# Optimization experiments

Measured on AMD Instinct MI355X. Metric: run time of the kernel, lower is better.

## Reference

```python
import jax, jax.numpy as jnp
import numpy as np

NUM_BINS = 16
BOUND = 3.0
MIN_BIN_WIDTH = 0.001
MIN_BIN_HEIGHT = 0.001
MIN_DERIVATIVE = 0.001
MIN_LAMBDA = 0.025
EPS = 1e-06


def setup_inputs() -> dict:
    key = jax.random.key(0)
    k1, k2 = jax.random.split(key)
    inputs = jax.random.normal(k1, (16384, 64), dtype=jnp.float32)
    params_unnorm = jax.random.normal(k2, (16384, 64, 4 * NUM_BINS - 1), dtype=jnp.float32)
    return {"inputs": inputs, "params_unnorm": params_unnorm}


def _calculate_knots(lengths, lower, upper):
    knots = jnp.cumsum(lengths, axis=-1) * (upper - lower) + lower
    pad = jnp.full(knots.shape[:-1] + (1,), lower, dtype=knots.dtype)
    knots = jnp.concatenate([pad, knots], axis=-1)
    knots = knots.at[..., -1].set(upper)
    lengths = jnp.diff(knots, axis=-1)
    return lengths, knots


def _spline_forward(inputs, params_unnorm):
    K = NUM_BINS
    w, h, d, lam = jnp.split(params_unnorm, [K, 2 * K, 3 * K - 1], axis=-1)
    w = jax.nn.softmax(w, axis=-1)
    h = jax.nn.softmax(h, axis=-1)
    d = jax.nn.softplus(d)
    lam = jax.nn.sigmoid(lam)

    widths = MIN_BIN_WIDTH + (1.0 - MIN_BIN_WIDTH * K) * w
    heights = MIN_BIN_HEIGHT + (1.0 - MIN_BIN_HEIGHT * K) * h
    derivatives = MIN_DERIVATIVE + d
    lambdas = (1.0 - 2.0 * MIN_LAMBDA) * lam + MIN_LAMBDA

    widths, cumwidths = _calculate_knots(widths, -BOUND, BOUND)
    heights, cumheights = _calculate_knots(heights, -BOUND, BOUND)
    # pad derivatives on both sides with 1 - min_derivative (boundary slopes == 1 after +min_derivative math in torch code semantics)
    edge = jnp.full(derivatives.shape[:-1] + (1,), 1.0 - MIN_DERIVATIVE, dtype=derivatives.dtype)
    derivatives = jnp.concatenate([edge, derivatives, edge], axis=-1)  # [..., K+1]

    # bin search: searchsorted(cumwidths + eps, x, right=True) - 1
    bin_idx = jnp.sum((cumwidths + EPS) <= inputs[..., None], axis=-1) - 1
    idx = jnp.clip(bin_idx, 0, K - 1)[..., None]

    def sel(x):
        return jnp.take_along_axis(x, idx, axis=-1)[..., 0]

    input_widths = sel(widths)
    input_heights = sel(heights)
    input_delta = input_heights / input_widths
    input_cumwidths = sel(cumwidths)
    input_cumheights = sel(cumheights)
    input_derivatives = sel(derivatives)
    input_derivatives_plus_one = sel(derivatives[..., 1:])
    input_lambdas = sel(lambdas)

    wb = jnp.sqrt(input_derivatives / input_derivatives_plus_one)
    lwa = input_lambdas
    lwb = input_lambdas * wb
    wc = (lwa * input_derivatives + (wb - lwb) * input_derivatives_plus_one) / input_delta
    ya = input_cumheights
    yb = input_heights + input_cumheights
    l1 = 1.0 - input_lambdas
    yc = (lwb * yb + l1 * ya) / (l1 + lwb)

    waya = ya
    wbyb = wb * yb
    wcyc = wc * yc
    theta = (inputs - input_cumwidths) / input_widths
    indicator = theta <= input_lambdas
    ltheta = input_lambdas - theta
    wcyctheta = wcyc * theta
    numerator = jnp.where(indicator, wcyctheta + waya * ltheta, (wcyc - wcyctheta) - wbyb * ltheta)
    wctheta = wc * theta
    denominator = jnp.where(indicator, wctheta + ltheta, (wc - wctheta) - wb * ltheta)
    outputs = numerator / denominator
    derivative_numerator = wc * jnp.where(
        indicator, input_lambdas * (yc - ya), (wb - lwb) * (yb - yc)
    ) / input_widths
    logabsdet = jnp.log(derivative_numerator) - 2.0 * jnp.log(jnp.abs(denominator))

    outside = (inputs < -BOUND) | (inputs > BOUND)
    outputs = jnp.where(outside, inputs, outputs)
    logabsdet = jnp.where(outside, 0.0, logabsdet)
    return outputs, logabsdet


def reference(inputs, params_unnorm):
    return _spline_forward(inputs, params_unnorm)
```

## Files before the change

### kernel.cpp

```cpp
#include <hip/hip_runtime.h>
#include <math.h>

#define NBINS 16
#define BOUNDV 3.0f
#define MIN_W 0.001f
#define MIN_H 0.001f
#define MIN_D 0.001f
#define MIN_L 0.025f
#define EPSV 1e-6f

#define TPB 128
#define PPE 63
#define SLABDW (TPB * PPE)
#define NVEC (SLABDW / 4)
#define TAILV (NVEC - 15 * TPB)

__device__ __forceinline__ float frcp(float v) { return __builtin_amdgcn_rcpf(v); }

__device__ __forceinline__ void load_slab(float4* v, const float* __restrict__ params,
                                          int s, int tid) {
    const float4* __restrict__ src = (const float4*)(params + (size_t)s * SLABDW);
    #pragma unroll
    for (int k = 0; k < 15; ++k) v[k] = src[tid + k * TPB];
    if (tid < TAILV) v[15] = src[tid + 15 * TPB];
}

__device__ __forceinline__ void store_slab(float* b, int tid, const float4* v) {
    float4* dst = (float4*)b;
    #pragma unroll
    for (int k = 0; k < 15; ++k) dst[tid + k * TPB] = v[k];
    if (tid < TAILV) dst[tid + 15 * TPB] = v[15];
}

__global__ __launch_bounds__(TPB) void lrs_kernel(
    const float* __restrict__ x_in,
    const float* __restrict__ params,
    float* __restrict__ out,
    int n)
{
    __shared__ __align__(16) float buf0[SLABDW];
    __shared__ __align__(16) float buf1[SLABDW];
    const int tid = threadIdx.x;
    const int nslab = n / TPB;
    const int g = gridDim.x;

    int s = blockIdx.x;
    if (s >= nslab) return;

    float4 v[16];
    load_slab(v, params, s, tid);
    float xc = x_in[(size_t)s * TPB + tid];
    store_slab(buf0, tid, v);
    __syncthreads();

    float* cur = buf0;
    float* nxt = buf1;

    for (; s < nslab; s += g) {
        const int sn = s + g;
        const bool hn = (sn < nslab);
        float xn = 0.f;
        if (hn) {
            load_slab(v, params, sn, tid);
            xn = x_in[(size_t)sn * TPB + tid];
        }

        const float* p = cur + tid * PPE;
        const float x = xc;

        float wv[NBINS];
        float mw = -1e30f;
        #pragma unroll
        for (int i = 0; i < NBINS; ++i) { wv[i] = p[i]; mw = fmaxf(mw, wv[i]); }
        float sw = 0.f;
        #pragma unroll
        for (int i = 0; i < NBINS; ++i) { wv[i] = __expf(wv[i] - mw); sw += wv[i]; }
        const float invw = frcp(sw);

        float cum = 0.f, knp = -BOUNDV, cw = -BOUNDV, cwn = 0.f;
        int bin = 0;
        #pragma unroll
        for (int i = 0; i < NBINS; ++i) {
            cum += fmaf(0.984f, wv[i] * invw, MIN_W);
            float kn = (i == NBINS - 1) ? BOUNDV : fmaf(6.f, cum, -BOUNDV);
            bool hit = (knp + EPSV <= x);
            if (i == 0) { cwn = kn; }
            else if (hit) { bin = i; cw = knp; cwn = kn; }
            knp = kn;
        }

        const float draw_lo = p[31 + bin];
        const float draw_hi = p[32 + bin];
        const float lraw    = p[47 + bin];

        float hv[NBINS];
        float mh = -1e30f;
        #pragma unroll
        for (int i = 0; i < NBINS; ++i) { hv[i] = p[16 + i]; mh = fmaxf(mh, hv[i]); }
        float sh = 0.f;
        #pragma unroll
        for (int i = 0; i < NBINS; ++i) { hv[i] = __expf(hv[i] - mh); sh += hv[i]; }
        const float invh = frcp(sh);

        float cumh = 0.f, khp = -BOUNDV, ya = -BOUNDV, yb = 0.f;
        #pragma unroll
        for (int i = 0; i < NBINS; ++i) {
            cumh += fmaf(0.984f, hv[i] * invh, MIN_H);
            float kh = (i == NBINS - 1) ? BOUNDV : fmaf(6.f, cumh, -BOUNDV);
            if (i == bin) { ya = khp; yb = kh; }
            khp = kh;
        }

        const float sp_lo = fmaxf(draw_lo, 0.f) + __logf(1.f + __expf(-fabsf(draw_lo)));
        const float sp_hi = fmaxf(draw_hi, 0.f) + __logf(1.f + __expf(-fabsf(draw_hi)));
        const float d_k  = (bin == 0)         ? (1.f - MIN_D) : (MIN_D + sp_lo);
        const float d_k1 = (bin == NBINS - 1) ? (1.f - MIN_D) : (MIN_D + sp_hi);

        const float sig = frcp(1.f + __expf(-lraw));
        const float lam = fmaf(1.f - 2.f * MIN_L, sig, MIN_L);

        const float width  = cwn - cw;
        const float height = yb - ya;
        const float inv_w  = frcp(width);
        const float inv_dl = width * frcp(height);

        const float wb  = __builtin_amdgcn_sqrtf(d_k * frcp(d_k1));
        const float lwb = lam * wb;
        const float wc  = (lam * d_k + (wb - lwb) * d_k1) * inv_dl;
        const float l1  = 1.f - lam;
        const float yc  = (lwb * yb + l1 * ya) * frcp(l1 + lwb);

        const float theta = (x - cw) * inv_w;
        const bool  ind   = (theta <= lam);
        const float lt    = lam - theta;

        const float wcyc  = wc * yc;
        const float wcyct = wcyc * theta;
        const float num   = ind ? fmaf(ya, lt, wcyct)
                                : (wcyc - wcyct) - (wb * yb) * lt;
        const float wct   = wc * theta;
        const float den   = ind ? (wct + lt)
                                : (wc - wct) - wb * lt;
        float outv = num * frcp(den);

        const float dnum = wc * (ind ? lam * (yc - ya) : (wb - lwb) * (yb - yc)) * inv_w;
        float lad = __logf(dnum) - 2.f * __logf(fabsf(den));

        const bool outside = (x < -BOUNDV) | (x > BOUNDV);
        outv = outside ? x   : outv;
        lad  = outside ? 0.f : lad;

        const size_t gid = (size_t)s * TPB + tid;
        out[gid]     = outv;
        out[n + gid] = lad;

        if (hn) store_slab(nxt, tid, v);
        __syncthreads();
        float* t = cur; cur = nxt; nxt = t;
        xc = xn;
    }
}

extern "C" void kernel_launch(void* const* d_in, const int* in_sizes, int n_in,
                              void* d_out, int out_size, void* d_ws, size_t ws_size,
                              hipStream_t stream) {
    const float* x      = (const float*)d_in[0];
    const float* params = (const float*)d_in[1];
    float* out          = (float*)d_out;
    const int n = in_sizes[0];
    const int blocks = 512;
    lrs_kernel<<<blocks, TPB, 0, stream>>>(x, params, out, n);
}
```

Baseline: 400.5 us.

## Use direct global-to-LDS loads and one-slab-per-block grid instead of persistent double buffering

The persistent double-buffered loop is replaced by a kernel that launches one block per 128-element slab. Each block copies its parameters straight from global memory into LDS with global_load_lds, skipping the register staging pass. The goal is more memory-level parallelism from many resident blocks and no register pressure from the float4 staging array. In exchange there is no explicit overlap inside a block, which relies on occupancy across blocks, and the LDS destination addressing of the wave-wide load intrinsic must be exactly right.

```diff
diff --git a/kernel.cpp b/kernel.cpp
--- a/kernel.cpp
+++ b/kernel.cpp
@@ -11,26 +11,14 @@
 
 #define TPB 128
 #define PPE 63
-#define SLABDW (TPB * PPE)
-#define NVEC (SLABDW / 4)
-#define TAILV (NVEC - 15 * TPB)
+#define NVEC (TPB * PPE / 4)
 
 __device__ __forceinline__ float frcp(float v) { return __builtin_amdgcn_rcpf(v); }
 
-__device__ __forceinline__ void load_slab(float4* v, const float* __restrict__ params,
-                                          int s, int tid) {
-    const float4* __restrict__ src = (const float4*)(params + (size_t)s * SLABDW);
-    #pragma unroll
-    for (int k = 0; k < 15; ++k) v[k] = src[tid + k * TPB];
-    if (tid < TAILV) v[15] = src[tid + 15 * TPB];
-}
-
-__device__ __forceinline__ void store_slab(float* b, int tid, const float4* v) {
-    float4* dst = (float4*)b;
-    #pragma unroll
-    for (int k = 0; k < 15; ++k) dst[tid + k * TPB] = v[k];
-    if (tid < TAILV) dst[tid + 15 * TPB] = v[15];
-}
+#define GLOAD_LDS16(gp, lp)                                             \
+    __builtin_amdgcn_global_load_lds(                                   \
+        (const __attribute__((address_space(1))) void*)(gp),            \
+        (__attribute__((address_space(3))) void*)(lp), 16, 0, 0)
 
 __global__ __launch_bounds__(TPB) void lrs_kernel(
     const float* __restrict__ x_in,
@@ -38,127 +26,111 @@
     float* __restrict__ out,
     int n)
 {
-    __shared__ __align__(16) float buf0[SLABDW];
-    __shared__ __align__(16) float buf1[SLABDW];
+    __shared__ __align__(16) float4 slab[NVEC];
     const int tid = threadIdx.x;
-    const int nslab = n / TPB;
-    const int g = gridDim.x;
+    const size_t gid = (size_t)blockIdx.x * TPB + tid;
 
-    int s = blockIdx.x;
-    if (s >= nslab) return;
+    const float x = x_in[gid];
 
-    float4 v[16];
-    load_slab(v, params, s, tid);
-    float xc = x_in[(size_t)s * TPB + tid];
-    store_slab(buf0, tid, v);
+    {
+        const float4* __restrict__ src =
+            (const float4*)(params + (size_t)blockIdx.x * (TPB * PPE));
+        #pragma unroll
+        for (int k = 0; k < 15; ++k) {
+            const int j = k * TPB + tid;
+            GLOAD_LDS16(src + j, &slab[j & ~63]);
+        }
+        const int j = 15 * TPB + tid;
+        if (j < NVEC) GLOAD_LDS16(src + j, &slab[j & ~63]);
+    }
     __syncthreads();
 
-    float* cur = buf0;
-    float* nxt = buf1;
+    const float* p = (const float*)slab + tid * PPE;
 
-    for (; s < nslab; s += g) {
-        const int sn = s + g;
-        const bool hn = (sn < nslab);
-        float xn = 0.f;
-        if (hn) {
-            load_slab(v, params, sn, tid);
-            xn = x_in[(size_t)sn * TPB + tid];
-        }
+    float wv[NBINS];
+    float mw = -1e30f;
+    #pragma unroll
+    for (int i = 0; i < NBINS; ++i) { wv[i] = p[i]; mw = fmaxf(mw, wv[i]); }
+    float sw = 0.f;
+    #pragma unroll
+    for (int i = 0; i < NBINS; ++i) { wv[i] = __expf(wv[i] - mw); sw += wv[i]; }
+    const float invw = frcp(sw);
 
-        const float* p = cur + tid * PPE;
-        const float x = xc;
+    float cum = 0.f, knp = -BOUNDV, cw = -BOUNDV, cwn = 0.f;
+    int bin = 0;
+    #pragma unroll
+    for (int i = 0; i < NBINS; ++i) {
+        cum += fmaf(0.984f, wv[i] * invw, MIN_W);
+        float kn = (i == NBINS - 1) ? BOUNDV : fmaf(6.f, cum, -BOUNDV);
+        bool hit = (knp + EPSV <= x);
+        if (i == 0) { cwn = kn; }
+        else if (hit) { bin = i; cw = knp; cwn = kn; }
+        knp = kn;
+    }
 
-        float wv[NBINS];
-        float mw = -1e30f;
-        #pragma unroll
-        for (int i = 0; i < NBINS; ++i) { wv[i] = p[i]; mw = fmaxf(mw, wv[i]); }
-        float sw = 0.f;
-        #pragma unroll
-        for (int i = 0; i < NBINS; ++i) { wv[i] = __expf(wv[i] - mw); sw += wv[i]; }
-        const float invw = frcp(sw);
+    const float draw_lo = p[31 + bin];
+    const float draw_hi = p[32 + bin];
+    const float lraw    = p[47 + bin];
 
-        float cum = 0.f, knp = -BOUNDV, cw = -BOUNDV, cwn = 0.f;
-        int bin = 0;
-        #pragma unroll
-        for (int i = 0; i < NBINS; ++i) {
-            cum += fmaf(0.984f, wv[i] * invw, MIN_W);
-            float kn = (i == NBINS - 1) ? BOUNDV : fmaf(6.f, cum, -BOUNDV);
-            bool hit = (knp + EPSV <= x);
-            if (i == 0) { cwn = kn; }
-            else if (hit) { bin = i; cw = knp; cwn = kn; }
-            knp = kn;
-        }
+    float hv[NBINS];
+    float mh = -1e30f;
+    #pragma unroll
+    for (int i = 0; i < NBINS; ++i) { hv[i] = p[16 + i]; mh = fmaxf(mh, hv[i]); }
+    float sh = 0.f;
+    #pragma unroll
+    for (int i = 0; i < NBINS; ++i) { hv[i] = __expf(hv[i] - mh); sh += hv[i]; }
+    const float invh = frcp(sh);
 
-        const float draw_lo = p[31 + bin];
-        const float draw_hi = p[32 + bin];
-        const float lraw    = p[47 + bin];
+    float cumh = 0.f, khp = -BOUNDV, ya = -BOUNDV, yb = 0.f;
+    #pragma unroll
+    for (int i = 0; i < NBINS; ++i) {
+        cumh += fmaf(0.984f, hv[i] * invh, MIN_H);
+        float kh = (i == NBINS - 1) ? BOUNDV : fmaf(6.f, cumh, -BOUNDV);
+        if (i == bin) { ya = khp; yb = kh; }
+        khp = kh;
+    }
 
-        float hv[NBINS];
-        float mh = -1e30f;
-        #pragma unroll
-        for (int i = 0; i < NBINS; ++i) { hv[i] = p[16 + i]; mh = fmaxf(mh, hv[i]); }
-        float sh = 0.f;
-        #pragma unroll
-        for (int i = 0; i < NBINS; ++i) { hv[i] = __expf(hv[i] - mh); sh += hv[i]; }
-        const float invh = frcp(sh);
+    const float sp_lo = fmaxf(draw_lo, 0.f) + __logf(1.f + __expf(-fabsf(draw_lo)));
+    const float sp_hi = fmaxf(draw_hi, 0.f) + __logf(1.f + __expf(-fabsf(draw_hi)));
+    const float d_k  = (bin == 0)         ? (1.f - MIN_D) : (MIN_D + sp_lo);
+    const float d_k1 = (bin == NBINS - 1) ? (1.f - MIN_D) : (MIN_D + sp_hi);
 
-        float cumh = 0.f, khp = -BOUNDV, ya = -BOUNDV, yb = 0.f;
-        #pragma unroll
-        for (int i = 0; i < NBINS; ++i) {
-            cumh += fmaf(0.984f, hv[i] * invh, MIN_H);
-            float kh = (i == NBINS - 1) ? BOUNDV : fmaf(6.f, cumh, -BOUNDV);
-            if (i == bin) { ya = khp; yb = kh; }
-            khp = kh;
-        }
+    const float sig = frcp(1.f + __expf(-lraw));
+    const float lam = fmaf(1.f - 2.f * MIN_L, sig, MIN_L);
 
-        const float sp_lo = fmaxf(draw_lo, 0.f) + __logf(1.f + __expf(-fabsf(draw_lo)));
-        const float sp_hi = fmaxf(draw_hi, 0.f) + __logf(1.f + __expf(-fabsf(draw_hi)));
-        const float d_k  = (bin == 0)         ? (1.f - MIN_D) : (MIN_D + sp_lo);
-        const float d_k1 = (bin == NBINS - 1) ? (1.f - MIN_D) : (MIN_D + sp_hi);
+    const float width  = cwn - cw;
+    const float height = yb - ya;
+    const float inv_w  = frcp(width);
+    const float inv_dl = width * frcp(height);
 
-        const float sig = frcp(1.f + __expf(-lraw));
-        const float lam = fmaf(1.f - 2.f * MIN_L, sig, MIN_L);
+    const float wb  = __builtin_amdgcn_sqrtf(d_k * frcp(d_k1));
+    const float lwb = lam * wb;
+    const float wc  = (lam * d_k + (wb - lwb) * d_k1) * inv_dl;
+    const float l1  = 1.f - lam;
+    const float yc  = (lwb * yb + l1 * ya) * frcp(l1 + lwb);
 
-        const float width  = cwn - cw;
-        const float height = yb - ya;
-        const float inv_w  = frcp(width);
-        const float inv_dl = width * frcp(height);
+    const float theta = (x - cw) * inv_w;
+    const bool  ind   = (theta <= lam);
+    const float lt    = lam - theta;
 
-        const float wb  = __builtin_amdgcn_sqrtf(d_k * frcp(d_k1));
-        const float lwb = lam * wb;
-        const float wc  = (lam * d_k + (wb - lwb) * d_k1) * inv_dl;
-        const float l1  = 1.f - lam;
-        const float yc  = (lwb * yb + l1 * ya) * frcp(l1 + lwb);
+    const float wcyc  = wc * yc;
+    const float wcyct = wcyc * theta;
+    const float num   = ind ? fmaf(ya, lt, wcyct)
+                            : (wcyc - wcyct) - (wb * yb) * lt;
+    const float wct   = wc * theta;
+    const float den   = ind ? (wct + lt)
+                            : (wc - wct) - wb * lt;
+    float outv = num * frcp(den);
 
-        const float theta = (x - cw) * inv_w;
-        const bool  ind   = (theta <= lam);
-        const float lt    = lam - theta;
+    const float dnum = wc * (ind ? lam * (yc - ya) : (wb - lwb) * (yb - yc)) * inv_w;
+    float lad = __logf(dnum) - 2.f * __logf(fabsf(den));
 
-        const float wcyc  = wc * yc;
-        const float wcyct = wcyc * theta;
-        const float num   = ind ? fmaf(ya, lt, wcyct)
-                                : (wcyc - wcyct) - (wb * yb) * lt;
-        const float wct   = wc * theta;
-        const float den   = ind ? (wct + lt)
-                                : (wc - wct) - wb * lt;
-        float outv = num * frcp(den);
+    const bool outside = (x < -BOUNDV) | (x > BOUNDV);
+    outv = outside ? x   : outv;
+    lad  = outside ? 0.f : lad;
 
-        const float dnum = wc * (ind ? lam * (yc - ya) : (wb - lwb) * (yb - yc)) * inv_w;
-        float lad = __logf(dnum) - 2.f * __logf(fabsf(den));
-
-        const bool outside = (x < -BOUNDV) | (x > BOUNDV);
-        outv = outside ? x   : outv;
-        lad  = outside ? 0.f : lad;
-
-        const size_t gid = (size_t)s * TPB + tid;
-        out[gid]     = outv;
-        out[n + gid] = lad;
-
-        if (hn) store_slab(nxt, tid, v);
-        __syncthreads();
-        float* t = cur; cur = nxt; nxt = t;
-        xc = xn;
-    }
+    out[gid]     = outv;
+    out[n + gid] = lad;
 }
 
 extern "C" void kernel_launch(void* const* d_in, const int* in_sizes, int n_in,
@@ -168,6 +140,6 @@
     const float* params = (const float*)d_in[1];
     float* out          = (float*)d_out;
     const int n = in_sizes[0];
-    const int blocks = 512;
+    const int blocks = n / TPB;
     lrs_kernel<<<blocks, TPB, 0, stream>>>(x, params, out, n);
 }
```

Result: faster. 354.3 us (-11.5%).
